# Optimization experiments

Measured on AMD Instinct MI355X. Metric: run time of the kernel, lower is better.

The kernel has to match this reference:

```python
import jax, jax.numpy as jnp
import numpy as np

N = 100000   # nodes
E = 1600000  # edges (avg degree 16)
IN, HID, OUT, HEADS = 8, 32, 16, 4


def setup_inputs() -> dict:
    key = jax.random.key(0)
    ks = jax.random.split(key, 12)
    def g(k, shape, fan):
        return (jax.random.normal(k, shape, jnp.float32) / np.float32(np.sqrt(fan)))
    x = jax.random.normal(ks[0], (N, IN), jnp.float32)
    edge_index = jax.random.randint(ks[1], (2, E), 0, N, dtype=jnp.int64)
    return {
        "x": x,
        "edge_index": edge_index,
        "W1": g(ks[2], (IN, HEADS * HID), IN),
        "att_src1": g(ks[3], (HEADS, HID), HID),
        "att_dst1": g(ks[4], (HEADS, HID), HID),
        "b1": jnp.zeros((HEADS * HID,), jnp.float32),
        "W2": g(ks[5], (HEADS * HID, OUT), HEADS * HID),
        "att_src2": g(ks[6], (1, OUT), OUT),
        "att_dst2": g(ks[7], (1, OUT), OUT),
        "b2": jnp.zeros((OUT,), jnp.float32),
        "Wc1": g(ks[8], (OUT, 8), OUT),
        "bc1": jnp.zeros((8,), jnp.float32),
        "Wc2": g(ks[9], (8, 1), 8),
        "bc2": jnp.zeros((1,), jnp.float32),
    }


def _gat_layer(x, W, att_src, att_dst, bias, src, dst, n, concat):
    """PyG GATConv (eval mode): gather -> per-edge attention -> segment softmax -> scatter."""
    H, D = att_src.shape
    h = (x @ W).reshape(n, H, D)                       # [N,H,D]
    a_s = jnp.einsum("nhd,hd->nh", h, att_src)          # [N,H]
    a_d = jnp.einsum("nhd,hd->nh", h, att_dst)          # [N,H]
    e = jax.nn.leaky_relu(a_s[src] + a_d[dst], 0.2)     # [Etot,H]
    m = jax.ops.segment_max(e, dst, num_segments=n)     # per-dst max for stable softmax
    m = jnp.where(jnp.isfinite(m), m, 0.0)
    e = jnp.exp(e - m[dst])
    denom = jax.ops.segment_sum(e, dst, num_segments=n)
    alpha = e / (denom[dst] + 1e-16)                    # [Etot,H]
    out = jax.ops.segment_sum(h[src] * alpha[:, :, None], dst, num_segments=n)  # [N,H,D]
    out = out.reshape(n, H * D) if concat else out.mean(axis=1)
    return out + bias


def reference(x, edge_index, W1, att_src1, att_dst1, b1, W2, att_src2, att_dst2, b2, Wc1, bc1, Wc2, bc2):
    n = x.shape[0]
    loops = jnp.arange(n, dtype=edge_index.dtype)       # add_self_loops=True (PyG default)
    src = jnp.concatenate([edge_index[0], loops])
    dst = jnp.concatenate([edge_index[1], loops])
    h = jax.nn.elu(_gat_layer(x, W1, att_src1, att_dst1, b1, src, dst, n, concat=True))
    emb = jax.nn.elu(_gat_layer(h, W2, att_src2, att_dst2, b2, src, dst, n, concat=False))
    risk = jax.nn.sigmoid(jax.nn.relu(emb @ Wc1 + bc1) @ Wc2 + bc2)
    return emb, risk
```

## Files before the change

### kernel.cpp

```cpp
#include <hip/hip_runtime.h>
#include <hip/hip_fp16.h>
#include <math.h>

#define N_NODES 100000
#define N_EDGES 1600000
#define F_IN 8
#define HID 32
#define HEADS 4
#define F1 128
#define F2 16
#define NB 391
#define NBLK_BIN 391
#define NBLK_A 391
#define BCAP 4864

__device__ __forceinline__ float leaky(float x){ return x > 0.f ? x : 0.2f * x; }
__device__ __forceinline__ float elu1(float x){ return x > 0.f ? x : __expf(x) - 1.f; }

__global__ __launch_bounds__(256) void k_bin_attn(
    const int* __restrict__ src, const int* __restrict__ dst,
    int* __restrict__ bucketCnt, unsigned int* __restrict__ ebuf,
    const float* __restrict__ x, const float* __restrict__ W1,
    const float* __restrict__ as1w, const float* __restrict__ ad1w,
    float* __restrict__ xa){
    __shared__ float smem[1344];
    int t = threadIdx.x;
    if (blockIdx.x < NBLK_BIN){
        int* hist    = (int*)smem;
        int* basePos = hist + NB;
        int* cur     = basePos + NB;
        for (int j = t; j < NB; j += 256) hist[j] = 0;
        __syncthreads();
        int base = blockIdx.x * 4096;
        int dv[16];
        #pragma unroll
        for (int j = 0; j < 16; j++){
            int e = base + j * 256 + t;
            dv[j] = (e < N_EDGES) ? dst[e] : -1;
            if (dv[j] >= 0) atomicAdd(&hist[dv[j] >> 8], 1);
        }
        __syncthreads();
        for (int j = t; j < NB; j += 256){
            int h = hist[j];
            if (h) basePos[j] = atomicAdd(&bucketCnt[j], h);
            cur[j] = 0;
        }
        __syncthreads();
        #pragma unroll
        for (int j = 0; j < 16; j++){
            if (dv[j] >= 0){
                int e = base + j * 256 + t;
                int d = dv[j];
                int b = d >> 8;
                int off = atomicAdd(&cur[b], 1);
                ebuf[b * BCAP + basePos[b] + off] = ((unsigned)(d & 255) << 17) | (unsigned)src[e];
            }
        }
    } else {
        float* W1s  = smem;
        float* atts = smem + 1024;
        float* attd = smem + 1152;
        float* cs   = smem + 1280;
        float* cd   = smem + 1312;
        ((float4*)W1s)[t] = ((const float4*)W1)[t];
        if (t < 128){ atts[t] = as1w[t]; attd[t] = ad1w[t]; }
        __syncthreads();
        if (t < 64){
            int m = t & 7, h = (t >> 3) & 3;
            bool sel = t >= 32;
            const float* wrow = W1s + m * F1 + h * 32;
            const float* av   = (sel ? attd : atts) + h * 32;
            float s = 0.f;
            #pragma unroll
            for (int d = 0; d < 32; d++) s += wrow[d] * av[d];
            (sel ? cd : cs)[h * 8 + m] = s;
        }
        __syncthreads();
        int n = (blockIdx.x - NBLK_BIN) * 256 + t;
        if (n < N_NODES){
            float4 x0 = ((const float4*)x)[n * 2];
            float4 x1 = ((const float4*)x)[n * 2 + 1];
            float4 osv, odv;
            float* po = (float*)&osv;
            float* pd = (float*)&odv;
            #pragma unroll
            for (int h = 0; h < 4; h++){
                const float* c0 = cs + h * 8;
                const float* c1 = cd + h * 8;
                po[h] = x0.x*c0[0] + x0.y*c0[1] + x0.z*c0[2] + x0.w*c0[3]
                      + x1.x*c0[4] + x1.y*c0[5] + x1.z*c0[6] + x1.w*c0[7];
                pd[h] = x0.x*c1[0] + x0.y*c1[1] + x0.z*c1[2] + x0.w*c1[3]
                      + x1.x*c1[4] + x1.y*c1[5] + x1.z*c1[6] + x1.w*c1[7];
            }
            float* px = xa + (size_t)n * 16;
            *(float4*)(px)      = x0;
            *(float4*)(px + 4)  = x1;
            *(float4*)(px + 8)  = osv;
            *(float4*)(px + 12) = odv;
        }
    }
}

__global__ __launch_bounds__(256) void k_local_csr(
    const int* __restrict__ bucketCnt, const unsigned int* __restrict__ ebuf,
    int* __restrict__ row_ptr, int* __restrict__ esrc){
    __shared__ int deg[256];
    __shared__ int scn[256];
    __shared__ int cntAll[NB];
    __shared__ unsigned int segs[BCAP];
    int b = blockIdx.x, t = threadIdx.x;
    deg[t] = 0;
    for (int j = t; j < NB; j += 256) cntAll[j] = bucketCnt[j];
    __syncthreads();
    int partial = 0;
    for (int j = t; j < b; j += 256) partial += cntAll[j];
    scn[t] = partial;
    __syncthreads();
    for (int off = 128; off > 0; off >>= 1){
        if (t < off) scn[t] += scn[t + off];
        __syncthreads();
    }
    int sbase = scn[0];
    int cnt = cntAll[b];
    __syncthreads();
    const unsigned int* seg = ebuf + b * BCAP;
    for (int i = t; i < cnt; i += 256){
        unsigned int e = seg[i];
        segs[i] = e;
        atomicAdd(&deg[e >> 17], 1);
    }
    __syncthreads();
    int v = deg[t];
    scn[t] = v;
    __syncthreads();
    for (int off = 1; off < 256; off <<= 1){
        int xx = (t >= off) ? scn[t - off] : 0;
        __syncthreads();
        scn[t] += xx;
        __syncthreads();
    }
    int excl = scn[t] - v;
    int start = sbase + excl;
    int n = b * 256 + t;
    if (n < N_NODES) row_ptr[n] = start;
    if (b == NB - 1 && t == 0) row_ptr[N_NODES] = sbase + cnt;
    deg[t] = start;
    __syncthreads();
    for (int i = t; i < cnt; i += 256){
        unsigned int e = segs[i];
        int pos = atomicAdd(&deg[e >> 17], 1);
        esrc[pos] = (int)(e & 0x1FFFFu);
    }
}

__global__ __launch_bounds__(256) void k_agg1(
    const float* __restrict__ xa, const int* __restrict__ row_ptr, const int* __restrict__ esrc,
    float* __restrict__ xagg, float* __restrict__ dden){
    int t = threadIdx.x;
    int wv = t >> 6, lane = t & 63;
    int n = blockIdx.x * 4 + wv;
    int g = lane >> 4;
    int l = lane & 15;
    int hd = l >> 2;
    int c2 = (l & 3) * 2;

    float vn = xa[(size_t)n * 16 + l];
    float adh = __shfl(vn, 12 + hd, 16);

    float den = 0.f, ac0 = 0.f, ac1 = 0.f;
    if (g == 0){
        float w = __expf(leaky(__shfl(vn, 8 + hd, 16) + adh));
        den = w;
        ac0 = w * __shfl(vn, c2, 16);
        ac1 = w * __shfl(vn, c2 + 1, 16);
    }
    int start = row_ptr[n], end = row_ptr[n + 1];
    int len = end - start;
    int chunk = (len + 3) >> 2;
    int i = start + g * chunk;
    int e = i + chunk; if (e > end) e = end;
    for (; i + 3 < e; i += 4){
        int s0 = esrc[i], s1 = esrc[i + 1], s2 = esrc[i + 2], s3 = esrc[i + 3];
        float v0 = xa[(size_t)s0 * 16 + l];
        float v1 = xa[(size_t)s1 * 16 + l];
        float v2 = xa[(size_t)s2 * 16 + l];
        float v3 = xa[(size_t)s3 * 16 + l];
        float w0 = __expf(leaky(__shfl(v0, 8 + hd, 16) + adh));
        float w1 = __expf(leaky(__shfl(v1, 8 + hd, 16) + adh));
        float w2 = __expf(leaky(__shfl(v2, 8 + hd, 16) + adh));
        float w3 = __expf(leaky(__shfl(v3, 8 + hd, 16) + adh));
        den += (w0 + w1) + (w2 + w3);
        ac0 = fmaf(w0, __shfl(v0, c2, 16), ac0); ac1 = fmaf(w0, __shfl(v0, c2 + 1, 16), ac1);
        ac0 = fmaf(w1, __shfl(v1, c2, 16), ac0); ac1 = fmaf(w1, __shfl(v1, c2 + 1, 16), ac1);
        ac0 = fmaf(w2, __shfl(v2, c2, 16), ac0); ac1 = fmaf(w2, __shfl(v2, c2 + 1, 16), ac1);
        ac0 = fmaf(w3, __shfl(v3, c2, 16), ac0); ac1 = fmaf(w3, __shfl(v3, c2 + 1, 16), ac1);
    }
    for (; i < e; i++){
        int s0 = esrc[i];
        float v0 = xa[(size_t)s0 * 16 + l];
        float w0 = __expf(leaky(__shfl(v0, 8 + hd, 16) + adh));
        den += w0;
        ac0 = fmaf(w0, __shfl(v0, c2, 16), ac0); ac1 = fmaf(w0, __shfl(v0, c2 + 1, 16), ac1);
    }
    den += __shfl_xor(den, 16); den += __shfl_xor(den, 32);
    ac0 += __shfl_xor(ac0, 16); ac0 += __shfl_xor(ac0, 32);
    ac1 += __shfl_xor(ac1, 16); ac1 += __shfl_xor(ac1, 32);

    if (lane < 16){
        float2 o; o.x = ac0; o.y = ac1;
        *(float2*)(xagg + (size_t)n * 32 + 2 * l) = o;
        if ((l & 3) == 0) dden[(size_t)n * 4 + hd] = den;
    }
}

__global__ __launch_bounds__(256) void k_epi(
    const float* __restrict__ xagg, const float* __restrict__ dden,
    const float* __restrict__ W1, const float* __restrict__ W2,
    const float* __restrict__ b1, const float* __restrict__ as2w, const float* __restrict__ ad2w,
    __half* __restrict__ h2h, float* __restrict__ a_s2, float* __restrict__ a_d2){
    __shared__ __half2 W1h[F_IN * 64];
    __shared__ __half2 W2t[F2 * 64];
    __shared__ __half2 hlsh[16 * 68];
    int t = threadIdx.x;
    {
        float4 w1v = ((const float4*)W1)[t];
        int m = t >> 5, j = (2 * t) & 63;
        W1h[m * 64 + j]     = __floats2half2_rn(w1v.x, w1v.y);
        W1h[m * 64 + j + 1] = __floats2half2_rn(w1v.z, w1v.w);
        #pragma unroll
        for (int hf = 0; hf < 2; hf++){
            int p = t + hf * 256;
            float4 wv = ((const float4*)W2)[p];
            int k = p >> 2, dbase = (p & 3) * 4;
            float vals[4] = {wv.x, wv.y, wv.z, wv.w};
            #pragma unroll
            for (int c = 0; c < 4; c++){
                int dw = (dbase + c) * 64 + (k >> 1);
                int sdw = dw ^ (((dw >> 6) & 7) << 2);
                ((__half*)W2t)[2 * sdw + (k & 1)] = __float2half(vals[c]);
            }
        }
    }
    __syncthreads();

    int nn = t >> 4, q = t & 15;
    int n = blockIdx.x * 16 + nn;
    int hd = q >> 2;

    const float* xg = xagg + (size_t)n * 32 + hd * 8;
    float4 xga = *(const float4*)(xg);
    float4 xgb = *(const float4*)(xg + 4);
    float invd = 1.f / dden[(size_t)n * 4 + hd];
    float xv[8] = {xga.x, xga.y, xga.z, xga.w, xgb.x, xgb.y, xgb.z, xgb.w};
    float pre[8] = {0,0,0,0,0,0,0,0};
    #pragma unroll
    for (int m = 0; m < 8; m++){
        float4 raw = *(const float4*)(W1h + m * 64 + 4 * q);
        const __half2* wp = (const __half2*)&raw;
        float xm = xv[m];
        float2 f0 = __half22float2(wp[0]);
        float2 f1 = __half22float2(wp[1]);
        float2 f2 = __half22float2(wp[2]);
        float2 f3 = __half22float2(wp[3]);
        pre[0] = fmaf(xm, f0.x, pre[0]); pre[1] = fmaf(xm, f0.y, pre[1]);
        pre[2] = fmaf(xm, f1.x, pre[2]); pre[3] = fmaf(xm, f1.y, pre[3]);
        pre[4] = fmaf(xm, f2.x, pre[4]); pre[5] = fmaf(xm, f2.y, pre[5]);
        pre[6] = fmaf(xm, f3.x, pre[6]); pre[7] = fmaf(xm, f3.y, pre[7]);
    }
    float4 ba = *(const float4*)(b1 + 8 * q);
    float4 bb = *(const float4*)(b1 + 8 * q + 4);
    __half2 hout[4];
    hout[0] = __floats2half2_rn(elu1(pre[0] * invd + ba.x), elu1(pre[1] * invd + ba.y));
    hout[1] = __floats2half2_rn(elu1(pre[2] * invd + ba.z), elu1(pre[3] * invd + ba.w));
    hout[2] = __floats2half2_rn(elu1(pre[4] * invd + bb.x), elu1(pre[5] * invd + bb.y));
    hout[3] = __floats2half2_rn(elu1(pre[6] * invd + bb.z), elu1(pre[7] * invd + bb.w));
    *(float4*)(hlsh + nn * 68 + 4 * q) = *(float4*)hout;
    __syncthreads();

    float dot = 0.f;
    #pragma unroll
    for (int ob = 0; ob < 8; ob++){
        __half2 acc2 = __float2half2_rn(0.f);
        #pragma unroll
        for (int kb = ob * 2; kb < ob * 2 + 2; kb++){
            float4 hr = *(const float4*)(hlsh + nn * 68 + 4 * kb);
            int dwb = 64 * q + 4 * kb;
            float4 wr = *(const float4*)(W2t + (dwb ^ (((dwb >> 6) & 7) << 2)));
            const __half2* hp  = (const __half2*)&hr;
            const __half2* wp2 = (const __half2*)&wr;
            acc2 = __hfma2(hp[0], wp2[0], acc2);
            acc2 = __hfma2(hp[1], wp2[1], acc2);
            acc2 = __hfma2(hp[2], wp2[2], acc2);
            acc2 = __hfma2(hp[3], wp2[3], acc2);
        }
        float2 fa = __half22float2(acc2);
        dot += fa.x + fa.y;
    }
    float ps = dot * as2w[q];
    float pd = dot * ad2w[q];
    #pragma unroll
    for (int off = 8; off >= 1; off >>= 1){
        ps += __shfl_down(ps, off, 16);
        pd += __shfl_down(pd, off, 16);
    }
    if (q == 0){ a_s2[n] = ps; a_d2[n] = pd; }
    h2h[(size_t)n * F2 + q] = __float2half(dot);
}

__global__ __launch_bounds__(256) void k_agg2(
    const __half* __restrict__ h2h, const float* __restrict__ a_s2, const float* __restrict__ a_d2,
    const int* __restrict__ row_ptr, const int* __restrict__ esrc,
    const float* __restrict__ b2, const float* __restrict__ Wc1, const float* __restrict__ bc1,
    const float* __restrict__ Wc2, const float* __restrict__ bc2, float* __restrict__ out){
    int t = threadIdx.x;
    int wv = t >> 6, lane = t & 63;
    int n = blockIdx.x * 4 + wv;
    int g = lane >> 3;
    int l = lane & 7;
    float adn = a_d2[n];
    const __half* hb2 = h2h + 2 * l;

    float den = 0.f, acc0 = 0.f, acc1 = 0.f;
    if (g == 0){
        float w = __expf(leaky(a_s2[n] + adn));
        den = w;
        float2 f = __half22float2(*(const __half2*)(hb2 + ((unsigned)n << 4)));
        acc0 = w * f.x; acc1 = w * f.y;
    }
    int start = row_ptr[n], end = row_ptr[n + 1];
    int len = end - start;
    int chunk = (len + 7) >> 3;
    int i = start + g * chunk;
    int e = i + chunk; if (e > end) e = end;
    for (int base = i; base < e; base += 4){
        bool v1 = base + 1 < e, v2 = base + 2 < e, v3 = base + 3 < e;
        int s0 = esrc[base];
        int s1 = v1 ? esrc[base + 1] : s0;
        int s2 = v2 ? esrc[base + 2] : s0;
        int s3 = v3 ? esrc[base + 3] : s0;
        float a0 = a_s2[s0], a1 = a_s2[s1], a2 = a_s2[s2], a3 = a_s2[s3];
        __half2 p0 = *(const __half2*)(hb2 + ((unsigned)s0 << 4));
        __half2 p1 = *(const __half2*)(hb2 + ((unsigned)s1 << 4));
        __half2 p2 = *(const __half2*)(hb2 + ((unsigned)s2 << 4));
        __half2 p3 = *(const __half2*)(hb2 + ((unsigned)s3 << 4));
        float w0 = __expf(leaky(a0 + adn));
        float w1 = v1 ? __expf(leaky(a1 + adn)) : 0.f;
        float w2 = v2 ? __expf(leaky(a2 + adn)) : 0.f;
        float w3 = v3 ? __expf(leaky(a3 + adn)) : 0.f;
        den += (w0 + w1) + (w2 + w3);
        float2 f0 = __half22float2(p0), f1 = __half22float2(p1);
        float2 f2 = __half22float2(p2), f3 = __half22float2(p3);
        acc0 += w0 * f0.x + w1 * f1.x + w2 * f2.x + w3 * f3.x;
        acc1 += w0 * f0.y + w1 * f1.y + w2 * f2.y + w3 * f3.y;
    }
    #pragma unroll
    for (int off = 8; off <= 32; off <<= 1){
        den  += __shfl_xor(den, off);
        acc0 += __shfl_xor(acc0, off);
        acc1 += __shfl_xor(acc1, off);
    }
    float inv = 1.f / (den + 1e-16f);
    float e0v = elu1(acc0 * inv + b2[2 * l]);
    float e1v = elu1(acc1 * inv + b2[2 * l + 1]);
    if (g == 0){
        float2 ov; ov.x = e0v; ov.y = e1v;
        *(float2*)(out + (size_t)n * 16 + 2 * l) = ov;
    }
    float hid = bc1[l];
    #pragma unroll
    for (int j = 0; j < 8; j++){
        float a = __shfl(e0v, j, 8);
        float b = __shfl(e1v, j, 8);
        hid += a * Wc1[(2 * j) * 8 + l] + b * Wc1[(2 * j + 1) * 8 + l];
    }
    float contrib = fmaxf(hid, 0.f) * Wc2[l];
    contrib += __shfl_xor(contrib, 1);
    contrib += __shfl_xor(contrib, 2);
    contrib += __shfl_xor(contrib, 4);
    if (lane == 0) out[(size_t)N_NODES * 16 + n] = 1.f / (1.f + __expf(-(contrib + bc2[0])));
}

extern "C" void kernel_launch(void* const* d_in, const int* in_sizes, int n_in,
                              void* d_out, int out_size, void* d_ws, size_t ws_size,
                              hipStream_t stream){
    const float* x    = (const float*)d_in[0];
    const int*   ei   = (const int*)d_in[1];
    const float* W1   = (const float*)d_in[2];
    const float* as1w = (const float*)d_in[3];
    const float* ad1w = (const float*)d_in[4];
    const float* b1   = (const float*)d_in[5];
    const float* W2   = (const float*)d_in[6];
    const float* as2w = (const float*)d_in[7];
    const float* ad2w = (const float*)d_in[8];
    const float* b2   = (const float*)d_in[9];
    const float* Wc1  = (const float*)d_in[10];
    const float* bc1  = (const float*)d_in[11];
    const float* Wc2  = (const float*)d_in[12];
    const float* bc2  = (const float*)d_in[13];
    float* out = (float*)d_out;
    const int* src = ei;
    const int* dst = ei + N_EDGES;

    float* ws   = (float*)d_ws;
    float* a_s2 = ws;
    float* a_d2 = a_s2 + N_NODES;
    float* xa   = a_d2 + N_NODES;
    float* xagg = xa + (size_t)N_NODES * 16;
    float* dden = xagg + (size_t)N_NODES * 32;
    __half* h2h = (__half*)(dden + (size_t)N_NODES * 4);
    int* bucketCnt = (int*)(h2h + (size_t)N_NODES * 16);
    int* row_ptr  = bucketCnt + NB;
    int* esrc     = row_ptr + N_NODES + 1;
    unsigned int* ebuf = (unsigned int*)(esrc + N_EDGES);

    hipMemsetAsync(bucketCnt, 0, NB * sizeof(int), stream);
    k_bin_attn<<<NBLK_BIN + NBLK_A, 256, 0, stream>>>(
        src, dst, bucketCnt, ebuf, x, W1, as1w, ad1w, xa);
    k_local_csr<<<NB, 256, 0, stream>>>(bucketCnt, ebuf, row_ptr, esrc);
    k_agg1<<<N_NODES / 4, 256, 0, stream>>>(xa, row_ptr, esrc, xagg, dden);
    k_epi<<<N_NODES / 16, 256, 0, stream>>>(
        xagg, dden, W1, W2, b1, as2w, ad2w, h2h, a_s2, a_d2);
    k_agg2<<<N_NODES / 4, 256, 0, stream>>>(h2h, a_s2, a_d2, row_ptr, esrc, b2, Wc1, bc1, Wc2, bc2, out);
}
```

Before: 242.1 us.

## Pack layer-2 features and attention scalars into one 64-byte row per node

k_epi now writes each node's 16 half-precision features packed as 8 floats, plus a_s2 and a_d2, into a single 16-float row. k_agg2 gathers that one row per neighbour with 16 lanes and extracts the values by shuffles, instead of doing separate scattered loads for a_s2 and the fp16 features. Its lane split changes from 8 groups of 8 to 4 groups of 16. k_agg1's tail loop is folded into the predicated 4-wide loop. This is meant to cut random-access memory transactions per edge, at the cost of more shuffles and six padding floats per row.

```diff
diff --git a/kernel.cpp b/kernel.cpp
--- a/kernel.cpp
+++ b/kernel.cpp
@@ -16,6 +16,10 @@
 
 __device__ __forceinline__ float leaky(float x){ return x > 0.f ? x : 0.2f * x; }
 __device__ __forceinline__ float elu1(float x){ return x > 0.f ? x : __expf(x) - 1.f; }
+__device__ __forceinline__ float half_of(float v, int hi){
+    float2 f = __half22float2(*(__half2*)&v);
+    return hi ? f.y : f.x;
+}
 
 __global__ __launch_bounds__(256) void k_bin_attn(
     const int* __restrict__ src, const int* __restrict__ dst,
@@ -179,29 +183,26 @@
     int chunk = (len + 3) >> 2;
     int i = start + g * chunk;
     int e = i + chunk; if (e > end) e = end;
-    for (; i + 3 < e; i += 4){
-        int s0 = esrc[i], s1 = esrc[i + 1], s2 = esrc[i + 2], s3 = esrc[i + 3];
+    for (int base = i; base < e; base += 4){
+        bool b1v = base + 1 < e, b2v = base + 2 < e, b3v = base + 3 < e;
+        int s0 = esrc[base];
+        int s1 = b1v ? esrc[base + 1] : s0;
+        int s2 = b2v ? esrc[base + 2] : s0;
+        int s3 = b3v ? esrc[base + 3] : s0;
         float v0 = xa[(size_t)s0 * 16 + l];
         float v1 = xa[(size_t)s1 * 16 + l];
         float v2 = xa[(size_t)s2 * 16 + l];
         float v3 = xa[(size_t)s3 * 16 + l];
         float w0 = __expf(leaky(__shfl(v0, 8 + hd, 16) + adh));
-        float w1 = __expf(leaky(__shfl(v1, 8 + hd, 16) + adh));
-        float w2 = __expf(leaky(__shfl(v2, 8 + hd, 16) + adh));
-        float w3 = __expf(leaky(__shfl(v3, 8 + hd, 16) + adh));
+        float w1 = b1v ? __expf(leaky(__shfl(v1, 8 + hd, 16) + adh)) : 0.f;
+        float w2 = b2v ? __expf(leaky(__shfl(v2, 8 + hd, 16) + adh)) : 0.f;
+        float w3 = b3v ? __expf(leaky(__shfl(v3, 8 + hd, 16) + adh)) : 0.f;
         den += (w0 + w1) + (w2 + w3);
         ac0 = fmaf(w0, __shfl(v0, c2, 16), ac0); ac1 = fmaf(w0, __shfl(v0, c2 + 1, 16), ac1);
         ac0 = fmaf(w1, __shfl(v1, c2, 16), ac0); ac1 = fmaf(w1, __shfl(v1, c2 + 1, 16), ac1);
         ac0 = fmaf(w2, __shfl(v2, c2, 16), ac0); ac1 = fmaf(w2, __shfl(v2, c2 + 1, 16), ac1);
         ac0 = fmaf(w3, __shfl(v3, c2, 16), ac0); ac1 = fmaf(w3, __shfl(v3, c2 + 1, 16), ac1);
     }
-    for (; i < e; i++){
-        int s0 = esrc[i];
-        float v0 = xa[(size_t)s0 * 16 + l];
-        float w0 = __expf(leaky(__shfl(v0, 8 + hd, 16) + adh));
-        den += w0;
-        ac0 = fmaf(w0, __shfl(v0, c2, 16), ac0); ac1 = fmaf(w0, __shfl(v0, c2 + 1, 16), ac1);
-    }
     den += __shfl_xor(den, 16); den += __shfl_xor(den, 32);
     ac0 += __shfl_xor(ac0, 16); ac0 += __shfl_xor(ac0, 32);
     ac1 += __shfl_xor(ac1, 16); ac1 += __shfl_xor(ac1, 32);
@@ -217,7 +218,7 @@
     const float* __restrict__ xagg, const float* __restrict__ dden,
     const float* __restrict__ W1, const float* __restrict__ W2,
     const float* __restrict__ b1, const float* __restrict__ as2w, const float* __restrict__ ad2w,
-    __half* __restrict__ h2h, float* __restrict__ a_s2, float* __restrict__ a_d2){
+    float* __restrict__ h2r){
     __shared__ __half2 W1h[F_IN * 64];
     __shared__ __half2 W2t[F2 * 64];
     __shared__ __half2 hlsh[16 * 68];
@@ -303,77 +304,74 @@
         ps += __shfl_down(ps, off, 16);
         pd += __shfl_down(pd, off, 16);
     }
-    if (q == 0){ a_s2[n] = ps; a_d2[n] = pd; }
-    h2h[(size_t)n * F2 + q] = __float2half(dot);
+    float dotp1 = __shfl_down(dot, 1, 16);
+    float psb = __shfl(ps, 0, 16);
+    float pdb = __shfl(pd, 0, 16);
+    float* rw = h2r + (size_t)n * 16;
+    if (!(q & 1)){
+        __half2 hp2 = __floats2half2_rn(dot, dotp1);
+        rw[q >> 1] = *(float*)&hp2;
+    }
+    if (q == 8) rw[8] = psb;
+    if (q == 9) rw[9] = pdb;
 }
 
 __global__ __launch_bounds__(256) void k_agg2(
-    const __half* __restrict__ h2h, const float* __restrict__ a_s2, const float* __restrict__ a_d2,
-    const int* __restrict__ row_ptr, const int* __restrict__ esrc,
+    const float* __restrict__ h2r, const int* __restrict__ row_ptr, const int* __restrict__ esrc,
     const float* __restrict__ b2, const float* __restrict__ Wc1, const float* __restrict__ bc1,
     const float* __restrict__ Wc2, const float* __restrict__ bc2, float* __restrict__ out){
     int t = threadIdx.x;
     int wv = t >> 6, lane = t & 63;
     int n = blockIdx.x * 4 + wv;
-    int g = lane >> 3;
-    int l = lane & 7;
-    float adn = a_d2[n];
-    const __half* hb2 = h2h + 2 * l;
-
-    float den = 0.f, acc0 = 0.f, acc1 = 0.f;
+    int g = lane >> 4;
+    int l = lane & 15;
+    int hsel = l >> 1, hpar = l & 1;
+
+    float vn = h2r[(size_t)n * 16 + l];
+    float adn = __shfl(vn, 9, 16);
+
+    float den = 0.f, acc = 0.f;
     if (g == 0){
-        float w = __expf(leaky(a_s2[n] + adn));
+        float w = __expf(leaky(__shfl(vn, 8, 16) + adn));
         den = w;
-        float2 f = __half22float2(*(const __half2*)(hb2 + ((unsigned)n << 4)));
-        acc0 = w * f.x; acc1 = w * f.y;
+        acc = w * half_of(__shfl(vn, hsel, 16), hpar);
     }
     int start = row_ptr[n], end = row_ptr[n + 1];
     int len = end - start;
-    int chunk = (len + 7) >> 3;
+    int chunk = (len + 3) >> 2;
     int i = start + g * chunk;
     int e = i + chunk; if (e > end) e = end;
     for (int base = i; base < e; base += 4){
-        bool v1 = base + 1 < e, v2 = base + 2 < e, v3 = base + 3 < e;
+        bool b1v = base + 1 < e, b2v = base + 2 < e, b3v = base + 3 < e;
         int s0 = esrc[base];
-        int s1 = v1 ? esrc[base + 1] : s0;
-        int s2 = v2 ? esrc[base + 2] : s0;
-        int s3 = v3 ? esrc[base + 3] : s0;
-        float a0 = a_s2[s0], a1 = a_s2[s1], a2 = a_s2[s2], a3 = a_s2[s3];
-        __half2 p0 = *(const __half2*)(hb2 + ((unsigned)s0 << 4));
-        __half2 p1 = *(const __half2*)(hb2 + ((unsigned)s1 << 4));
-        __half2 p2 = *(const __half2*)(hb2 + ((unsigned)s2 << 4));
-        __half2 p3 = *(const __half2*)(hb2 + ((unsigned)s3 << 4));
-        float w0 = __expf(leaky(a0 + adn));
-        float w1 = v1 ? __expf(leaky(a1 + adn)) : 0.f;
-        float w2 = v2 ? __expf(leaky(a2 + adn)) : 0.f;
-        float w3 = v3 ? __expf(leaky(a3 + adn)) : 0.f;
+        int s1 = b1v ? esrc[base + 1] : s0;
+        int s2 = b2v ? esrc[base + 2] : s0;
+        int s3 = b3v ? esrc[base + 3] : s0;
+        float v0 = h2r[(size_t)s0 * 16 + l];
+        float v1 = h2r[(size_t)s1 * 16 + l];
+        float v2 = h2r[(size_t)s2 * 16 + l];
+        float v3 = h2r[(size_t)s3 * 16 + l];
+        float w0 = __expf(leaky(__shfl(v0, 8, 16) + adn));
+        float w1 = b1v ? __expf(leaky(__shfl(v1, 8, 16) + adn)) : 0.f;
+        float w2 = b2v ? __expf(leaky(__shfl(v2, 8, 16) + adn)) : 0.f;
+        float w3 = b3v ? __expf(leaky(__shfl(v3, 8, 16) + adn)) : 0.f;
         den += (w0 + w1) + (w2 + w3);
-        float2 f0 = __half22float2(p0), f1 = __half22float2(p1);
-        float2 f2 = __half22float2(p2), f3 = __half22float2(p3);
-        acc0 += w0 * f0.x + w1 * f1.x + w2 * f2.x + w3 * f3.x;
-        acc1 += w0 * f0.y + w1 * f1.y + w2 * f2.y + w3 * f3.y;
-    }
+        acc = fmaf(w0, half_of(__shfl(v0, hsel, 16), hpar), acc);
+        acc = fmaf(w1, half_of(__shfl(v1, hsel, 16), hpar), acc);
+        acc = fmaf(w2, half_of(__shfl(v2, hsel, 16), hpar), acc);
+        acc = fmaf(w3, half_of(__shfl(v3, hsel, 16), hpar), acc);
+    }
+    den += __shfl_xor(den, 16); den += __shfl_xor(den, 32);
+    acc += __shfl_xor(acc, 16); acc += __shfl_xor(acc, 32);
+
+    float inv = 1.f / (den + 1e-16f);
+    float ev = elu1(acc * inv + b2[l]);
+    if (lane < 16) out[(size_t)n * 16 + l] = ev;
+    float hid = bc1[l & 7];
     #pragma unroll
-    for (int off = 8; off <= 32; off <<= 1){
-        den  += __shfl_xor(den, off);
-        acc0 += __shfl_xor(acc0, off);
-        acc1 += __shfl_xor(acc1, off);
-    }
-    float inv = 1.f / (den + 1e-16f);
-    float e0v = elu1(acc0 * inv + b2[2 * l]);
-    float e1v = elu1(acc1 * inv + b2[2 * l + 1]);
-    if (g == 0){
-        float2 ov; ov.x = e0v; ov.y = e1v;
-        *(float2*)(out + (size_t)n * 16 + 2 * l) = ov;
-    }
-    float hid = bc1[l];
-    #pragma unroll
-    for (int j = 0; j < 8; j++){
-        float a = __shfl(e0v, j, 8);
-        float b = __shfl(e1v, j, 8);
-        hid += a * Wc1[(2 * j) * 8 + l] + b * Wc1[(2 * j + 1) * 8 + l];
-    }
-    float contrib = fmaxf(hid, 0.f) * Wc2[l];
+    for (int d = 0; d < 16; d++)
+        hid += __shfl(ev, d, 16) * Wc1[d * 8 + (l & 7)];
+    float contrib = fmaxf(hid, 0.f) * Wc2[l & 7];
     contrib += __shfl_xor(contrib, 1);
     contrib += __shfl_xor(contrib, 2);
     contrib += __shfl_xor(contrib, 4);
@@ -402,13 +400,11 @@
     const int* dst = ei + N_EDGES;
 
     float* ws   = (float*)d_ws;
-    float* a_s2 = ws;
-    float* a_d2 = a_s2 + N_NODES;
-    float* xa   = a_d2 + N_NODES;
+    float* xa   = ws;
     float* xagg = xa + (size_t)N_NODES * 16;
     float* dden = xagg + (size_t)N_NODES * 32;
-    __half* h2h = (__half*)(dden + (size_t)N_NODES * 4);
-    int* bucketCnt = (int*)(h2h + (size_t)N_NODES * 16);
+    float* h2r  = dden + (size_t)N_NODES * 4;
+    int* bucketCnt = (int*)(h2r + (size_t)N_NODES * 16);
     int* row_ptr  = bucketCnt + NB;
     int* esrc     = row_ptr + N_NODES + 1;
     unsigned int* ebuf = (unsigned int*)(esrc + N_EDGES);
@@ -419,6 +415,6 @@
     k_local_csr<<<NB, 256, 0, stream>>>(bucketCnt, ebuf, row_ptr, esrc);
     k_agg1<<<N_NODES / 4, 256, 0, stream>>>(xa, row_ptr, esrc, xagg, dden);
     k_epi<<<N_NODES / 16, 256, 0, stream>>>(
-        xagg, dden, W1, W2, b1, as2w, ad2w, h2h, a_s2, a_d2);
-    k_agg2<<<N_NODES / 4, 256, 0, stream>>>(h2h, a_s2, a_d2, row_ptr, esrc, b2, Wc1, bc1, Wc2, bc2, out);
-}
+        xagg, dden, W1, W2, b1, as2w, ad2w, h2r);
+    k_agg2<<<N_NODES / 4, 256, 0, stream>>>(h2r, row_ptr, esrc, b2, Wc1, bc1, Wc2, bc2, out);
+}
```

Result: no change. 242.8 us (+0.3%).
